# Performance work log

Hardware: AMD Instinct MI355X
Metric: run time of the kernel (lower is better)

Reference implementation:

```python
import jax, jax.numpy as jnp
import numpy as np

D_HIDDEN = 1024
NUM_HEADS = 16
D_HEAD = D_HIDDEN // NUM_HEADS


def setup_inputs() -> dict:
    key = jax.random.key(0)
    ks = jax.random.split(key, 9)
    N, S, D = 4, 2048, D_HIDDEN
    s = 1.0 / np.sqrt(D)
    inp = {
        "x": jax.random.normal(ks[0], (N, S, D), dtype=jnp.float32),
        "Wq": jax.random.uniform(ks[1], (D, D), jnp.float32, -s, s),
        "bq": jnp.zeros((D,), jnp.float32),
        "Wk": jax.random.uniform(ks[2], (D, D), jnp.float32, -s, s),
        "bk": jnp.zeros((D,), jnp.float32),
        "Wv": jax.random.uniform(ks[3], (D, D), jnp.float32, -s, s),
        "bv": jnp.zeros((D,), jnp.float32),
        "Wo": jax.random.uniform(ks[4], (D, D), jnp.float32, -s, s),
        "bo": jnp.zeros((D,), jnp.float32),
        "ln_gamma": jnp.ones((D,), jnp.float32),
        "ln_beta": jnp.zeros((D,), jnp.float32),
    }
    return inp


def _layer_norm(x, gamma, beta, eps=1e-5):
    mu = jnp.mean(x, axis=-1, keepdims=True)
    var = jnp.var(x, axis=-1, keepdims=True)
    return (x - mu) * jax.lax.rsqrt(var + eps) * gamma + beta


def reference(x, Wq, bq, Wk, bk, Wv, bv, Wo, bo, ln_gamma, ln_beta):
    N, S, D = x.shape
    H, Dh = NUM_HEADS, D_HEAD
    xn = _layer_norm(x, ln_gamma, ln_beta)
    # torch Linear: y = x @ W.T + b
    q = (xn @ Wq.T + bq).reshape(N, S, H, Dh)
    k = (xn @ Wk.T + bk).reshape(N, S, H, Dh)
    v = (xn @ Wv.T + bv).reshape(N, S, H, Dh)
    # scores: [N, H, S, S]
    scores = jnp.einsum('nxhd,nyhd->nhxy', q, k) / np.sqrt(Dh)
    # causal mask: positions y > x get -inf
    mask = jnp.triu(jnp.full((S, S), -jnp.inf, dtype=scores.dtype), k=1)
    attn = jax.nn.softmax(scores + mask[None, None], axis=-1)
    z = jnp.einsum('nhxy,nyhd->nxhd', attn, v).reshape(N, S, D)
    return z @ Wo.T + bo
```

## Files before the change

kernel.cpp:

```cpp
#include <hip/hip_runtime.h>

typedef unsigned short u16;
typedef unsigned int   u32;
typedef __bf16 bf16x8 __attribute__((ext_vector_type(8)));
typedef float  f32x4  __attribute__((ext_vector_type(4)));
typedef unsigned short u16x8 __attribute__((ext_vector_type(8)));
typedef unsigned short u16x4 __attribute__((ext_vector_type(4)));

#define SEQ 2048
#define DM  1024
#define TOKS 8388608
#define SCLQ 0.18033688f

__device__ __forceinline__ float bf2f(u16 u) {
    u32 i = ((u32)u) << 16;
    float f; __builtin_memcpy(&f, &i, 4); return f;
}
__device__ __forceinline__ u16 f2bf(float f) {
    u32 i; __builtin_memcpy(&i, &f, 4);
    return (u16)((i + 0x7FFFu + ((i >> 16) & 1u)) >> 16);
}
__device__ __forceinline__ bf16x8 ld8(const u16* p) {
    return __builtin_bit_cast(bf16x8, *(const u16x8*)p);
}
#define GLD16(src, dst) __builtin_amdgcn_global_load_lds( \
    (const __attribute__((address_space(1))) void*)(src), \
    (__attribute__((address_space(3))) void*)(dst), 16, 0, 0)

__device__ __forceinline__ int sniff_fp32(const u32* x) {
    u32 w = x[threadIdx.x & 63];
    int e0 = (int)((w >> 7) & 0xFFu);
    int cnt = (e0 >= 100 && e0 <= 140) ? 1 : 0;
#pragma unroll
    for (int off = 32; off; off >>= 1) cnt += __shfl_xor(cnt, off);
    return cnt < 32;
}

__global__ __launch_bounds__(256) void prep_k(const void* __restrict__ x,
                                              const void* Wq, const void* Wk, const void* Wv, const void* Wo,
                                              const void* bq, const void* bk, const void* bv, const void* bo,
                                              const void* g, const void* b,
                                              u16* __restrict__ dstW, u16* __restrict__ dstV,
                                              u16* __restrict__ xn, int* __restrict__ flagp) {
    const int bid = blockIdx.x, tid = threadIdx.x;
    const int fp32m = sniff_fp32((const u32*)x);

    if (bid < 8192) {
        const int row = bid;
        float f[4], s1 = 0.f, s2 = 0.f;
        if (fp32m) {
            f32x4 v = *(const f32x4*)((const float*)x + (size_t)row * DM + tid * 4);
#pragma unroll
            for (int j = 0; j < 4; ++j) f[j] = v[j];
        } else {
            u16x4 v = *(const u16x4*)((const u16*)x + (size_t)row * DM + tid * 4);
#pragma unroll
            for (int j = 0; j < 4; ++j) f[j] = bf2f(v[j]);
        }
#pragma unroll
        for (int j = 0; j < 4; ++j) { s1 += f[j]; s2 += f[j] * f[j]; }
#pragma unroll
        for (int off = 32; off; off >>= 1) { s1 += __shfl_xor(s1, off); s2 += __shfl_xor(s2, off); }
        __shared__ float red[8];
        const int wave = tid >> 6, lane = tid & 63;
        if (lane == 0) { red[wave] = s1; red[4 + wave] = s2; }
        __syncthreads();
        s1 = red[0] + red[1] + red[2] + red[3];
        s2 = red[4] + red[5] + red[6] + red[7];
        const float mu = s1 * (1.f / DM);
        const float var = s2 * (1.f / DM) - mu * mu;
        const float rs = rsqrtf(var + 1e-5f);
        float gv[4], bv2[4];
        if (fp32m) {
            f32x4 gg = *(const f32x4*)((const float*)g + tid * 4);
            f32x4 bb = *(const f32x4*)((const float*)b + tid * 4);
#pragma unroll
            for (int j = 0; j < 4; ++j) { gv[j] = gg[j]; bv2[j] = bb[j]; }
        } else {
            u16x4 gg = *(const u16x4*)((const u16*)g + tid * 4);
            u16x4 bb = *(const u16x4*)((const u16*)b + tid * 4);
#pragma unroll
            for (int j = 0; j < 4; ++j) { gv[j] = bf2f(gg[j]); bv2[j] = bf2f(bb[j]); }
        }
        u16x4 o;
#pragma unroll
        for (int j = 0; j < 4; ++j) o[j] = f2bf((f[j] - mu) * rs * gv[j] + bv2[j]);
        *(u16x4*)(xn + (size_t)row * DM + tid * 4) = o;
    } else if (bid < 12288) {
        const int wi = (bid - 8192) >> 10, blk = (bid - 8192) & 1023;
        const void* src = (wi == 0) ? Wq : (wi == 1) ? Wk : (wi == 2) ? Wv : Wo;
        const size_t off = (size_t)blk * 1024 + tid * 4;
        u16x4 o;
        if (fp32m) {
            const float* f = (const float*)src + off;
#pragma unroll
            for (int j = 0; j < 4; ++j) o[j] = f2bf(f[j]);
        } else {
            o = *(const u16x4*)((const u16*)src + off);
        }
        *(u16x4*)(dstW + (size_t)wi * 1048576 + off) = o;
    } else {
#pragma unroll
        for (int i = 0; i < 4; ++i) {
            const void* src = (i == 0) ? bq : (i == 1) ? bk : (i == 2) ? bv : bo;
            u16x4 o;
            if (fp32m) {
                const float* f = (const float*)src + tid * 4;
#pragma unroll
                for (int j = 0; j < 4; ++j) o[j] = f2bf(f[j]);
            } else {
                o = *(const u16x4*)((const u16*)src + tid * 4);
            }
            *(u16x4*)(dstV + (size_t)i * 1024 + tid * 4) = o;
        }
        if (tid == 0) *flagp = fp32m;
    }
}

template <int VT>
__device__ __forceinline__ void gemm_core(u16* As, u16* Bs,
                                          const u16* __restrict__ A,
                                          const u16* __restrict__ W,
                                          const u16* __restrict__ bias,
                                          u16* __restrict__ out,
                                          float scale) {
    const int tid = threadIdx.x, wave = tid >> 6, lane = tid & 63;
    const int l4 = lane & 15, q4 = lane >> 4;
    const int bm = blockIdx.x, bn = blockIdx.y;
    const int wm = (wave >> 1) * 64, wn = (wave & 1) * 64;
    f32x4 acc[4][4] = {};
    const int srow = wave * 32 + (lane >> 2);
    const int skoff = (lane & 3) * 8;
    const u16* Ag = A + ((size_t)(bm * 128 + srow)) * DM + skoff;
    const u16* Wg = W + ((size_t)(bn * 128 + srow)) * DM + skoff;
    u16* As0 = As + wave * 1024;
    u16* Bs0 = Bs + wave * 1024;

    for (int k0 = 0; k0 < DM; k0 += 32) {
        GLD16(Ag + k0, As0);
        GLD16(Ag + 16 * DM + k0, As0 + 512);
        GLD16(Wg + k0, Bs0);
        GLD16(Wg + 16 * DM + k0, Bs0 + 512);
        __syncthreads();
        bf16x8 af[4], bfr[4];
#pragma unroll
        for (int t = 0; t < 4; ++t)
            af[t] = ld8(As + (wm + t * 16 + l4) * 32 + q4 * 8);
#pragma unroll
        for (int t = 0; t < 4; ++t)
            bfr[t] = ld8(Bs + (wn + t * 16 + l4) * 32 + q4 * 8);
#pragma unroll
        for (int mt = 0; mt < 4; ++mt)
#pragma unroll
            for (int nt = 0; nt < 4; ++nt)
                acc[mt][nt] = __builtin_amdgcn_mfma_f32_16x16x32_bf16(af[mt], bfr[nt], acc[mt][nt], 0, 0, 0);
        __syncthreads();
    }

#pragma unroll
    for (int nt = 0; nt < 4; ++nt) {
        const int col = bn * 128 + wn + nt * 16 + l4;
        const float bs = bf2f(bias[col]);
#pragma unroll
        for (int mt = 0; mt < 4; ++mt) {
            const int row0 = bm * 128 + wm + mt * 16 + q4 * 4;
            if (VT == 1) {
                const int nb = row0 >> 11, s0 = row0 & 2047;
                u16x4 pk;
#pragma unroll
                for (int r = 0; r < 4; ++r) pk[r] = f2bf((acc[mt][nt][r] + bs) * scale);
                *(u16x4*)(out + ((size_t)(nb * 1024 + col)) * SEQ + s0) = pk;
            } else {
#pragma unroll
                for (int r = 0; r < 4; ++r)
                    out[(size_t)(row0 + r) * DM + col] = f2bf((acc[mt][nt][r] + bs) * scale);
            }
        }
    }
}

__global__ __launch_bounds__(256) void gemm_qkv_k(const u16* __restrict__ xn, const u16* __restrict__ Wc,
                                                  const u16* __restrict__ Vc,
                                                  u16* __restrict__ Q, u16* __restrict__ K, u16* __restrict__ Vt) {
    __shared__ alignas(16) u16 As[128 * 32];
    __shared__ alignas(16) u16 Bs[128 * 32];
    const int z = blockIdx.z;
    if (z == 0)      gemm_core<0>(As, Bs, xn, Wc,               Vc,        Q,  SCLQ);
    else if (z == 1) gemm_core<0>(As, Bs, xn, Wc + 1048576,     Vc + 1024, K,  1.0f);
    else             gemm_core<1>(As, Bs, xn, Wc + 2 * 1048576, Vc + 2048, Vt, 1.0f);
}

__global__ __launch_bounds__(512) void gemm_out_k(const u16* __restrict__ Z, const u16* __restrict__ Wc,
                                                  const u16* __restrict__ Vc,
                                                  u16* __restrict__ out, const int* __restrict__ flagp) {
    __shared__ alignas(16) u16 As[128 * 32];
    __shared__ alignas(16) u16 Bs[128 * 32];
    const u16* W = Wc + 3 * 1048576;
    const u16* bias = Vc + 3 * 1024;
    const int tid = threadIdx.x, wave = tid >> 6, lane = tid & 63;
    const int l4 = lane & 15, q4 = lane >> 4;
    const int bm = blockIdx.x, bn = blockIdx.y;
    const int wm = (wave >> 2) * 64, wn = (wave & 3) * 32;
    const int fp32m = *flagp;
    f32x4 acc[4][2] = {};
    const int srow = (wave & 3) * 32 + (lane >> 2);
    const int skoff = (lane & 3) * 8;
    const u16* Sg = (wave < 4) ? (Z + ((size_t)(bm * 128 + srow)) * DM + skoff)
                               : (W + ((size_t)(bn * 128 + srow)) * DM + skoff);
    u16* dst0 = (wave < 4) ? (As + (wave & 3) * 1024) : (Bs + (wave & 3) * 1024);

    for (int k0 = 0; k0 < DM; k0 += 32) {
        GLD16(Sg + k0, dst0);
        GLD16(Sg + 16 * DM + k0, dst0 + 512);
        __syncthreads();
        bf16x8 af[4], bfr[2];
#pragma unroll
        for (int t = 0; t < 4; ++t)
            af[t] = ld8(As + (wm + t * 16 + l4) * 32 + q4 * 8);
#pragma unroll
        for (int t = 0; t < 2; ++t)
            bfr[t] = ld8(Bs + (wn + t * 16 + l4) * 32 + q4 * 8);
#pragma unroll
        for (int mt = 0; mt < 4; ++mt)
#pragma unroll
            for (int nt = 0; nt < 2; ++nt)
                acc[mt][nt] = __builtin_amdgcn_mfma_f32_16x16x32_bf16(af[mt], bfr[nt], acc[mt][nt], 0, 0, 0);
        __syncthreads();
    }

#pragma unroll
    for (int nt = 0; nt < 2; ++nt) {
        const int col = bn * 128 + wn + nt * 16 + l4;
        const float bs = bf2f(bias[col]);
#pragma unroll
        for (int mt = 0; mt < 4; ++mt) {
            const int row0 = bm * 128 + wm + mt * 16 + q4 * 4;
            if (fp32m) {
#pragma unroll
                for (int r = 0; r < 4; ++r)
                    ((float*)out)[(size_t)(row0 + r) * DM + col] = acc[mt][nt][r] + bs;
            } else {
#pragma unroll
                for (int r = 0; r < 4; ++r)
                    out[(size_t)(row0 + r) * DM + col] = f2bf(acc[mt][nt][r] + bs);
            }
        }
    }
}

__global__ __launch_bounds__(256, 4) void flash_k(const u16* __restrict__ Q,
                                                  const u16* __restrict__ K,
                                                  const u16* __restrict__ Vt,
                                                  u16* __restrict__ Z) {
    const int bh = blockIdx.x;
    const int qb = 15 - (int)blockIdx.y;
    const int n = bh >> 4, h = bh & 15;
    const int tid = threadIdx.x, wave = tid >> 6, lane = tid & 63;
    const int l4 = lane & 15, q4 = lane >> 4;

    __shared__ alignas(16) u16 Ks[2][64 * 32];
    __shared__ alignas(16) u16 Vs[2][64 * 32];
    __shared__ alignas(16) u16 Pl[4][2][16 * 72];

    const int Q0w = qb * 128 + wave * 32;
    bf16x8 qf[2][2];
#pragma unroll
    for (int qt = 0; qt < 2; ++qt) {
        const u16* Qr = Q + ((size_t)(n * SEQ + Q0w + qt * 16 + l4)) * DM + h * 64 + q4 * 8;
        qf[qt][0] = ld8(Qr);
        qf[qt][1] = ld8(Qr + 32);
    }

    const int srow = lane >> 2, scol = (lane & 3) * 8;
    const u16* Kg = K + ((size_t)(n * SEQ + wave * 16 + srow)) * DM + h * 64 + scol;
    const u16* Vg = Vt + ((size_t)(n * 1024 + h * 64 + wave * 16 + srow)) * SEQ + scol;
    u16* KsD0 = &Ks[0][wave * 512];
    u16* KsD1 = &Ks[1][wave * 512];
    u16* VsD0 = &Vs[0][wave * 512];
    u16* VsD1 = &Vs[1][wave * 512];

    f32x4 o[2][4] = {};
    float l_acc[2] = {0.f, 0.f};
    const int nch = 2 * qb + 2;

    for (int c = 0; c < nch; ++c) {
        const int kv0 = c * 64;
        const size_t krow = (size_t)kv0 * DM;
        GLD16(Kg + krow, KsD0);
        GLD16(Kg + krow + 32, KsD1);
        GLD16(Vg + kv0, VsD0);
        GLD16(Vg + kv0 + 32, VsD1);
        __syncthreads();

        bf16x8 a[4][2];
#pragma unroll
        for (int mt = 0; mt < 4; ++mt) {
            a[mt][0] = ld8(&Ks[0][(mt * 16 + l4) * 32 + q4 * 8]);
            a[mt][1] = ld8(&Ks[1][(mt * 16 + l4) * 32 + q4 * 8]);
        }
#pragma unroll
        for (int qt = 0; qt < 2; ++qt) {
            f32x4 st[4];
#pragma unroll
            for (int mt = 0; mt < 4; ++mt) {
                f32x4 zz = {0.f, 0.f, 0.f, 0.f};
                st[mt] = __builtin_amdgcn_mfma_f32_16x16x32_bf16(a[mt][0], qf[qt][0], zz, 0, 0, 0);
                st[mt] = __builtin_amdgcn_mfma_f32_16x16x32_bf16(a[mt][1], qf[qt][1], st[mt], 0, 0, 0);
            }
            const int qg = Q0w + qt * 16 + l4;
            u16* P = Pl[wave][qt];
            float la = l_acc[qt];
#pragma unroll
            for (int mt = 0; mt < 4; ++mt) {
                __bf16 pk[4];
#pragma unroll
                for (int r = 0; r < 4; ++r) {
                    const int kv = kv0 + mt * 16 + q4 * 4 + r;
                    float p = __builtin_amdgcn_exp2f(st[mt][r]);
                    p = (kv > qg) ? 0.f : p;
                    la += p;
                    pk[r] = (__bf16)p;
                }
                *(u16x4*)(P + l4 * 72 + mt * 16 + q4 * 4) = *(u16x4*)pk;
            }
            l_acc[qt] = la;
        }
#pragma unroll
        for (int ks = 0; ks < 2; ++ks) {
            bf16x8 pf0 = ld8(&Pl[wave][0][l4 * 72 + ks * 32 + q4 * 8]);
            bf16x8 pf1 = ld8(&Pl[wave][1][l4 * 72 + ks * 32 + q4 * 8]);
#pragma unroll
            for (int nt = 0; nt < 4; ++nt) {
                bf16x8 vf = ld8(&Vs[ks][(nt * 16 + l4) * 32 + q4 * 8]);
                o[0][nt] = __builtin_amdgcn_mfma_f32_16x16x32_bf16(pf0, vf, o[0][nt], 0, 0, 0);
                o[1][nt] = __builtin_amdgcn_mfma_f32_16x16x32_bf16(pf1, vf, o[1][nt], 0, 0, 0);
            }
        }
        __syncthreads();
    }

#pragma unroll
    for (int qt = 0; qt < 2; ++qt) {
        float l = l_acc[qt];
        l += __shfl_xor(l, 16);
        l += __shfl_xor(l, 32);
        float lr[4];
#pragma unroll
        for (int r = 0; r < 4; ++r) lr[r] = 1.f / __shfl(l, q4 * 4 + r);
#pragma unroll
        for (int nt = 0; nt < 4; ++nt) {
            const int col = h * 64 + nt * 16 + l4;
#pragma unroll
            for (int r = 0; r < 4; ++r) {
                const int row = n * SEQ + Q0w + qt * 16 + q4 * 4 + r;
                Z[(size_t)row * DM + col] = f2bf(o[qt][nt][r] * lr[r]);
            }
        }
    }
}

extern "C" void kernel_launch(void* const* d_in, const int* in_sizes, int n_in,
                              void* d_out, int out_size, void* d_ws, size_t ws_size,
                              hipStream_t stream) {
    const void* x  = d_in[0];
    const void* Wq = d_in[1];
    const void* bq = d_in[2];
    const void* Wk = d_in[3];
    const void* bk = d_in[4];
    const void* Wv = d_in[5];
    const void* bv = d_in[6];
    const void* Wo = d_in[7];
    const void* bo = d_in[8];
    const void* g  = d_in[9];
    const void* b  = d_in[10];
    u16* ws = (u16*)d_ws;

    u16* xn  = ws;
    u16* Qb  = ws + (size_t)TOKS;
    u16* Kb  = ws + (size_t)2 * TOKS;
    u16* Vtb = ws + (size_t)3 * TOKS;
    u16* Zb  = ws;
    u16* Wc  = ws + (size_t)4 * TOKS;
    u16* Vc  = Wc + 4 * 1048576;
    int* flagp = (int*)(Vc + 8 * 1024);

    prep_k<<<dim3(12289), 256, 0, stream>>>(x, Wq, Wk, Wv, Wo, bq, bk, bv, bo, g, b, Wc, Vc, xn, flagp);
    gemm_qkv_k<<<dim3(64, 8, 3), 256, 0, stream>>>(xn, Wc, Vc, Qb, Kb, Vtb);
    flash_k<<<dim3(64, 16), 256, 0, stream>>>(Qb, Kb, Vtb, Zb);
    gemm_out_k<<<dim3(64, 8), 512, 0, stream>>>(Zb, Wc, Vc, (u16*)d_out, flagp);
}
```

Measured before the change: 259.4 us.

## Enlarge flash attention query tile and skip weight copy in bf16 mode

The flash kernel now processes 256 query rows per block (64 per wave) instead of 128, so each K/V tile loaded into shared memory is reused across four query sub-tiles. Fully masked sub-tiles are skipped, and unmasked chunks take a mask-free softmax path. Blocks are ordered to pair long and short causal ranges. Separately, in bf16 input mode the weight copy in prep is skipped and the GEMMs read the original weights directly. The larger tile raises register pressure and lowers occupancy (launch bounds 4 to 2), and leaves only half as many blocks.

```diff
diff --git a/kernel.cpp b/kernel.cpp
--- a/kernel.cpp
+++ b/kernel.cpp
@@ -87,17 +87,14 @@
         for (int j = 0; j < 4; ++j) o[j] = f2bf((f[j] - mu) * rs * gv[j] + bv2[j]);
         *(u16x4*)(xn + (size_t)row * DM + tid * 4) = o;
     } else if (bid < 12288) {
+        if (!fp32m) return;
         const int wi = (bid - 8192) >> 10, blk = (bid - 8192) & 1023;
         const void* src = (wi == 0) ? Wq : (wi == 1) ? Wk : (wi == 2) ? Wv : Wo;
         const size_t off = (size_t)blk * 1024 + tid * 4;
+        const float* f = (const float*)src + off;
         u16x4 o;
-        if (fp32m) {
-            const float* f = (const float*)src + off;
-#pragma unroll
-            for (int j = 0; j < 4; ++j) o[j] = f2bf(f[j]);
-        } else {
-            o = *(const u16x4*)((const u16*)src + off);
-        }
+#pragma unroll
+        for (int j = 0; j < 4; ++j) o[j] = f2bf(f[j]);
         *(u16x4*)(dstW + (size_t)wi * 1048576 + off) = o;
     } else {
 #pragma unroll
@@ -181,27 +178,37 @@
 
 __global__ __launch_bounds__(256) void gemm_qkv_k(const u16* __restrict__ xn, const u16* __restrict__ Wc,
                                                   const u16* __restrict__ Vc,
+                                                  const void* Wq, const void* Wk, const void* Wv,
+                                                  const int* __restrict__ flagp,
                                                   u16* __restrict__ Q, u16* __restrict__ K, u16* __restrict__ Vt) {
     __shared__ alignas(16) u16 As[128 * 32];
     __shared__ alignas(16) u16 Bs[128 * 32];
     const int z = blockIdx.z;
-    if (z == 0)      gemm_core<0>(As, Bs, xn, Wc,               Vc,        Q,  SCLQ);
-    else if (z == 1) gemm_core<0>(As, Bs, xn, Wc + 1048576,     Vc + 1024, K,  1.0f);
-    else             gemm_core<1>(As, Bs, xn, Wc + 2 * 1048576, Vc + 2048, Vt, 1.0f);
+    const int fp32m = *flagp;
+    if (z == 0) {
+        const u16* W = fp32m ? Wc : (const u16*)Wq;
+        gemm_core<0>(As, Bs, xn, W, Vc, Q, SCLQ);
+    } else if (z == 1) {
+        const u16* W = fp32m ? (Wc + 1048576) : (const u16*)Wk;
+        gemm_core<0>(As, Bs, xn, W, Vc + 1024, K, 1.0f);
+    } else {
+        const u16* W = fp32m ? (Wc + 2 * 1048576) : (const u16*)Wv;
+        gemm_core<1>(As, Bs, xn, W, Vc + 2048, Vt, 1.0f);
+    }
 }
 
 __global__ __launch_bounds__(512) void gemm_out_k(const u16* __restrict__ Z, const u16* __restrict__ Wc,
-                                                  const u16* __restrict__ Vc,
+                                                  const u16* __restrict__ Vc, const void* Wo,
                                                   u16* __restrict__ out, const int* __restrict__ flagp) {
     __shared__ alignas(16) u16 As[128 * 32];
     __shared__ alignas(16) u16 Bs[128 * 32];
-    const u16* W = Wc + 3 * 1048576;
+    const int fp32m = *flagp;
+    const u16* W = fp32m ? (Wc + 3 * 1048576) : (const u16*)Wo;
     const u16* bias = Vc + 3 * 1024;
     const int tid = threadIdx.x, wave = tid >> 6, lane = tid & 63;
     const int l4 = lane & 15, q4 = lane >> 4;
     const int bm = blockIdx.x, bn = blockIdx.y;
     const int wm = (wave >> 2) * 64, wn = (wave & 3) * 32;
-    const int fp32m = *flagp;
     f32x4 acc[4][2] = {};
     const int srow = (wave & 3) * 32 + (lane >> 2);
     const int skoff = (lane & 3) * 8;
@@ -248,24 +255,25 @@
     }
 }
 
-__global__ __launch_bounds__(256, 4) void flash_k(const u16* __restrict__ Q,
+__global__ __launch_bounds__(256, 2) void flash_k(const u16* __restrict__ Q,
                                                   const u16* __restrict__ K,
                                                   const u16* __restrict__ Vt,
                                                   u16* __restrict__ Z) {
     const int bh = blockIdx.x;
-    const int qb = 15 - (int)blockIdx.y;
+    const int yy = (int)blockIdx.y;
+    const int qb = (yy < 4) ? yy : 11 - yy;
     const int n = bh >> 4, h = bh & 15;
     const int tid = threadIdx.x, wave = tid >> 6, lane = tid & 63;
     const int l4 = lane & 15, q4 = lane >> 4;
 
     __shared__ alignas(16) u16 Ks[2][64 * 32];
     __shared__ alignas(16) u16 Vs[2][64 * 32];
-    __shared__ alignas(16) u16 Pl[4][2][16 * 72];
-
-    const int Q0w = qb * 128 + wave * 32;
-    bf16x8 qf[2][2];
-#pragma unroll
-    for (int qt = 0; qt < 2; ++qt) {
+    __shared__ alignas(16) u16 Pl[4][4][16 * 72];
+
+    const int Q0w = qb * 256 + wave * 64;
+    bf16x8 qf[4][2];
+#pragma unroll
+    for (int qt = 0; qt < 4; ++qt) {
         const u16* Qr = Q + ((size_t)(n * SEQ + Q0w + qt * 16 + l4)) * DM + h * 64 + q4 * 8;
         qf[qt][0] = ld8(Qr);
         qf[qt][1] = ld8(Qr + 32);
@@ -279,9 +287,9 @@
     u16* VsD0 = &Vs[0][wave * 512];
     u16* VsD1 = &Vs[1][wave * 512];
 
-    f32x4 o[2][4] = {};
-    float l_acc[2] = {0.f, 0.f};
-    const int nch = 2 * qb + 2;
+    f32x4 o[4][4] = {};
+    float l_acc[4] = {0.f, 0.f, 0.f, 0.f};
+    const int nch = 4 * qb + 4;
 
     for (int c = 0; c < nch; ++c) {
         const int kv0 = c * 64;
@@ -299,7 +307,9 @@
             a[mt][1] = ld8(&Ks[1][(mt * 16 + l4) * 32 + q4 * 8]);
         }
 #pragma unroll
-        for (int qt = 0; qt < 2; ++qt) {
+        for (int qt = 0; qt < 4; ++qt) {
+            const int qbase = Q0w + qt * 16;
+            if (kv0 > qbase + 15) continue;
             f32x4 st[4];
 #pragma unroll
             for (int mt = 0; mt < 4; ++mt) {
@@ -307,40 +317,58 @@
                 st[mt] = __builtin_amdgcn_mfma_f32_16x16x32_bf16(a[mt][0], qf[qt][0], zz, 0, 0, 0);
                 st[mt] = __builtin_amdgcn_mfma_f32_16x16x32_bf16(a[mt][1], qf[qt][1], st[mt], 0, 0, 0);
             }
-            const int qg = Q0w + qt * 16 + l4;
             u16* P = Pl[wave][qt];
             float la = l_acc[qt];
-#pragma unroll
-            for (int mt = 0; mt < 4; ++mt) {
-                __bf16 pk[4];
-#pragma unroll
-                for (int r = 0; r < 4; ++r) {
-                    const int kv = kv0 + mt * 16 + q4 * 4 + r;
-                    float p = __builtin_amdgcn_exp2f(st[mt][r]);
-                    p = (kv > qg) ? 0.f : p;
-                    la += p;
-                    pk[r] = (__bf16)p;
+            if (kv0 + 63 <= qbase) {
+#pragma unroll
+                for (int mt = 0; mt < 4; ++mt) {
+                    __bf16 pk[4];
+#pragma unroll
+                    for (int r = 0; r < 4; ++r) {
+                        float p = __builtin_amdgcn_exp2f(st[mt][r]);
+                        la += p;
+                        pk[r] = (__bf16)p;
+                    }
+                    *(u16x4*)(P + l4 * 72 + mt * 16 + q4 * 4) = *(u16x4*)pk;
                 }
-                *(u16x4*)(P + l4 * 72 + mt * 16 + q4 * 4) = *(u16x4*)pk;
+            } else {
+                const int qg = qbase + l4;
+#pragma unroll
+                for (int mt = 0; mt < 4; ++mt) {
+                    __bf16 pk[4];
+#pragma unroll
+                    for (int r = 0; r < 4; ++r) {
+                        const int kv = kv0 + mt * 16 + q4 * 4 + r;
+                        float p = __builtin_amdgcn_exp2f(st[mt][r]);
+                        p = (kv > qg) ? 0.f : p;
+                        la += p;
+                        pk[r] = (__bf16)p;
+                    }
+                    *(u16x4*)(P + l4 * 72 + mt * 16 + q4 * 4) = *(u16x4*)pk;
+                }
             }
             l_acc[qt] = la;
         }
 #pragma unroll
         for (int ks = 0; ks < 2; ++ks) {
-            bf16x8 pf0 = ld8(&Pl[wave][0][l4 * 72 + ks * 32 + q4 * 8]);
-            bf16x8 pf1 = ld8(&Pl[wave][1][l4 * 72 + ks * 32 + q4 * 8]);
-#pragma unroll
-            for (int nt = 0; nt < 4; ++nt) {
-                bf16x8 vf = ld8(&Vs[ks][(nt * 16 + l4) * 32 + q4 * 8]);
-                o[0][nt] = __builtin_amdgcn_mfma_f32_16x16x32_bf16(pf0, vf, o[0][nt], 0, 0, 0);
-                o[1][nt] = __builtin_amdgcn_mfma_f32_16x16x32_bf16(pf1, vf, o[1][nt], 0, 0, 0);
-            }
-        }
-        __syncthreads();
-    }
-
-#pragma unroll
-    for (int qt = 0; qt < 2; ++qt) {
+            bf16x8 vf[4];
+#pragma unroll
+            for (int nt = 0; nt < 4; ++nt)
+                vf[nt] = ld8(&Vs[ks][(nt * 16 + l4) * 32 + q4 * 8]);
+#pragma unroll
+            for (int qt = 0; qt < 4; ++qt) {
+                if (kv0 > Q0w + qt * 16 + 15) continue;
+                bf16x8 pf = ld8(&Pl[wave][qt][l4 * 72 + ks * 32 + q4 * 8]);
+#pragma unroll
+                for (int nt = 0; nt < 4; ++nt)
+                    o[qt][nt] = __builtin_amdgcn_mfma_f32_16x16x32_bf16(pf, vf[nt], o[qt][nt], 0, 0, 0);
+            }
+        }
+        __syncthreads();
+    }
+
+#pragma unroll
+    for (int qt = 0; qt < 4; ++qt) {
         float l = l_acc[qt];
         l += __shfl_xor(l, 16);
         l += __shfl_xor(l, 32);
@@ -385,7 +413,7 @@
     int* flagp = (int*)(Vc + 8 * 1024);
 
     prep_k<<<dim3(12289), 256, 0, stream>>>(x, Wq, Wk, Wv, Wo, bq, bk, bv, bo, g, b, Wc, Vc, xn, flagp);
-    gemm_qkv_k<<<dim3(64, 8, 3), 256, 0, stream>>>(xn, Wc, Vc, Qb, Kb, Vtb);
-    flash_k<<<dim3(64, 16), 256, 0, stream>>>(Qb, Kb, Vtb, Zb);
-    gemm_out_k<<<dim3(64, 8), 512, 0, stream>>>(Zb, Wc, Vc, (u16*)d_out, flagp);
-}
+    gemm_qkv_k<<<dim3(64, 8, 3), 256, 0, stream>>>(xn, Wc, Vc, Wq, Wk, Wv, flagp, Qb, Kb, Vtb);
+    flash_k<<<dim3(64, 8), 256, 0, stream>>>(Qb, Kb, Vtb, Zb);
+    gemm_out_k<<<dim3(64, 8), 512, 0, stream>>>(Zb, Wc, Vc, Wo, (u16*)d_out, flagp);
+}
```

Measured after the change: 275.4 us. 6.2% more time.
